# Kernel tuning notes

Measured on AMD Instinct MI355X. Metric: run time of the kernel, lower is better.

The kernel has to match this reference:

```python
import jax, jax.numpy as jnp
import numpy as np

B, S, L = 8, 2048, 8
H, NH = 768, 12
DH = H // NH
NUM_REL = 100
LN_EPS = 1e-5


def setup_inputs() -> dict:
    key = jax.random.key(0)
    ks = jax.random.split(key, 16)
    inp = {
        'text_embeddings': jax.random.normal(ks[0], (B, S, H), dtype=jnp.float32),
        # values in [-1, 64); -1 marks 'no leaf' and is masked out
        'graph_structure': jax.random.randint(ks[1], (B, S, L), -1, 64, dtype=jnp.int64),
        'relation_ids': jax.random.randint(ks[2], (B, S, L), 0, NUM_REL, dtype=jnp.int64),
        'rel_table': jax.random.normal(ks[3], (NUM_REL, H), dtype=jnp.float32),
        'Wq': jax.random.normal(ks[4], (H, H), dtype=jnp.float32) / np.sqrt(H),
        'bq': jnp.zeros((H,), dtype=jnp.float32),
        'Wk': jax.random.normal(ks[5], (H, H), dtype=jnp.float32) / np.sqrt(H),
        'bk': jnp.zeros((H,), dtype=jnp.float32),
        'Wv': jax.random.normal(ks[6], (H, H), dtype=jnp.float32) / np.sqrt(H),
        'bv': jnp.zeros((H,), dtype=jnp.float32),
        'Wo': jax.random.normal(ks[7], (H, H), dtype=jnp.float32) / np.sqrt(H),
        'bo': jnp.zeros((H,), dtype=jnp.float32),
        'gamma': jnp.ones((H,), dtype=jnp.float32),
        'beta': jnp.zeros((H,), dtype=jnp.float32),
    }
    return inp


def reference(text_embeddings, graph_structure, relation_ids, rel_table,
              Wq, bq, Wk, bk, Wv, bv, Wo, bo, gamma, beta):
    b, s, h = text_embeddings.shape
    l = relation_ids.shape[2]
    # embedding gather (clamp -1 -> 0, masked later)
    rel_emb = rel_table[jnp.clip(relation_ids, 0, None)]  # [B,S,L,H]
    # projections; query has length-1 per root token
    q = (text_embeddings @ Wq + bq).reshape(b, s, NH, DH)          # [B,S,N,D]
    k = (rel_emb @ Wk + bk).reshape(b, s, l, NH, DH)               # [B,S,L,N,D]
    v = (rel_emb @ Wv + bv).reshape(b, s, l, NH, DH)
    scores = jnp.einsum('bsnd,bslnd->bsnl', q, k) / np.sqrt(DH)    # [B,S,N,L]
    mask = (graph_structure != -1)[:, :, None, :]                  # [B,S,1,L]
    scores = jnp.where(mask, scores, jnp.float32(-10000.0))
    probs = jax.nn.softmax(scores, axis=-1)                        # [B,S,N,L]
    ctx = jnp.einsum('bsnl,bslnd->bsnd', probs, v).reshape(b, s, h)
    out = ctx @ Wo + bo
    x = text_embeddings + out
    mu = jnp.mean(x, axis=-1, keepdims=True)
    var = jnp.mean(jnp.square(x - mu), axis=-1, keepdims=True)
    return (x - mu) * jax.lax.rsqrt(var + LN_EPS) * gamma + beta
```

## Files before the change

### kernel.cpp

```cpp
#include <hip/hip_runtime.h>
#include <hip/hip_bf16.h>

#define H 768
#define NH 12
#define DH 64
#define LL 8
#define NTOK 16384
#define NREL 100
#define NRELP 128
#define PADW 72

typedef __attribute__((ext_vector_type(8))) short short8;
typedef __attribute__((ext_vector_type(4))) float f32x4;

__device__ __forceinline__ float bf2f(ushort u) {
  union { unsigned int i; float f; } v; v.i = ((unsigned int)u) << 16; return v.f;
}
__device__ __forceinline__ float bflo(unsigned int u) {
  union { unsigned int i; float f; } v; v.i = u << 16; return v.f;
}
__device__ __forceinline__ float bfhi(unsigned int u) {
  union { unsigned int i; float f; } v; v.i = u & 0xffff0000u; return v.f;
}
__device__ __forceinline__ ushort f2bf(float f) {
  union { float f; unsigned int i; } v; v.f = f;
  unsigned int x = v.i;
  return (ushort)((x + 0x7fffu + ((x >> 16) & 1u)) >> 16);
}
__device__ __forceinline__ unsigned int cvt_pk_bf16(float lo, float hi) {
  unsigned int r;
  asm("v_cvt_pk_bf16_f32 %0, %1, %2" : "=v"(r) : "v"(lo), "v"(hi));
  return r;
}

__global__ __launch_bounds__(256) void prep_kernel(
    const float* __restrict__ s0, ushort* __restrict__ d0,
    const float* __restrict__ s1, ushort* __restrict__ d1,
    const float* __restrict__ s2, ushort* __restrict__ d2,
    const float* __restrict__ s3, ushort* __restrict__ d3,
    const float* __restrict__ rel, ushort* __restrict__ RelB) {
  if (blockIdx.z == 4) {
    int b = blockIdx.y * 24 + blockIdx.x;
    if (b < 96) {
      int i = (b * 256 + threadIdx.x) * 4;
      int row = i / H;
      ushort4 o = {0, 0, 0, 0};
      if (row < NREL) {
        float4 v = *(const float4*)(rel + i);
        o.x = f2bf(v.x); o.y = f2bf(v.y); o.z = f2bf(v.z); o.w = f2bf(v.w);
      }
      *(ushort4*)(RelB + i) = o;
    }
    return;
  }
  const float* src; ushort* dst;
  switch (blockIdx.z) {
    case 0:  src = s0; dst = d0; break;
    case 1:  src = s1; dst = d1; break;
    case 2:  src = s2; dst = d2; break;
    default: src = s3; dst = d3; break;
  }
  __shared__ float tile[32][33];
  int bx = blockIdx.x * 32, by = blockIdx.y * 32;
  int tx = threadIdx.x & 31, ty = threadIdx.x >> 5;
  #pragma unroll
  for (int i = 0; i < 32; i += 8)
    tile[ty + i][tx] = src[(size_t)(by + ty + i) * H + bx + tx];
  __syncthreads();
  #pragma unroll
  for (int i = 0; i < 32; i += 8)
    dst[(size_t)(bx + ty + i) * H + by + tx] = f2bf(tile[tx][ty + i]);
}

__device__ __forceinline__ void gload_lds16(const void* g, void* l) {
  __builtin_amdgcn_global_load_lds(
      (const __attribute__((address_space(1))) unsigned int*)g,
      (__attribute__((address_space(3))) unsigned int*)l, 16, 0, 0);
}

#define BM 128
#define BN 256
#define BK 64
#define ATILE (BM * BK)
#define BTILE (BN * BK)

#define GEMM_COMPUTE()                                                         \
  _Pragma("unroll")                                                            \
  for (int kk = 0; kk < 2; ++kk) {                                             \
    const int sw = (((kk << 2) | lk) ^ (lr & 7)) * 8;                          \
    short8 af[4], bfr[8];                                                      \
    _Pragma("unroll")                                                          \
    for (int m = 0; m < 4; ++m)                                                \
      af[m] = *(const short8*)(As + (wr * 64 + m * 16 + lr) * BK + sw);        \
    _Pragma("unroll")                                                          \
    for (int n = 0; n < 8; ++n)                                                \
      bfr[n] = *(const short8*)(Bs + (wc * 128 + n * 16 + lr) * BK + sw);      \
    _Pragma("unroll")                                                          \
    for (int m = 0; m < 4; ++m)                                                \
      _Pragma("unroll")                                                        \
      for (int n = 0; n < 8; ++n)                                              \
        acc[m][n] = __builtin_amdgcn_mfma_f32_16x16x32_bf16(af[m], bfr[n],     \
                                                            acc[m][n], 0, 0, 0);\
  }

#define GEMM_EPILOGUE()                                                        \
  _Pragma("unroll")                                                            \
  for (int m = 0; m < 4; ++m) {                                                \
    _Pragma("unroll")                                                          \
    for (int n = 0; n < 8; ++n) {                                              \
      int col = col0 + wc * 128 + n * 16 + lr;                                 \
      float b = bias[col];                                                     \
      _Pragma("unroll")                                                        \
      for (int j = 0; j < 4; ++j) {                                            \
        int row = row0 + wr * 64 + m * 16 + lk * 4 + j;                        \
        C[(size_t)row * N + col] = f2bf(acc[m][n][j] + b);                     \
      }                                                                        \
    }                                                                          \
  }

__device__ __forceinline__ void gemm_body(
    ushort* As, ushort* Bs,
    const ushort* __restrict__ A,
    const ushort* __restrict__ Bt,
    const float* __restrict__ bias,
    ushort* __restrict__ C,
    int M, int N, int K, int bx, int by) {
  const int tid = threadIdx.x;
  const int row0 = by * BM;
  const int col0 = bx * BN;
  const int wave = tid >> 6;
  const int lane = tid & 63;
  const int wr = wave >> 1, wc = wave & 1;
  const int lr = lane & 15, lk = lane >> 4;
  f32x4 acc[4][8];
  #pragma unroll
  for (int m = 0; m < 4; ++m)
    #pragma unroll
    for (int n = 0; n < 8; ++n) acc[m][n] = (f32x4)(0.f);

  for (int k0 = 0; k0 < K; k0 += BK) {
    #pragma unroll
    for (int i = 0; i < 4; ++i) {
      int c = tid + i * 256; int r = c >> 3, s = c & 7; int gsx = s ^ (r & 7);
      gload_lds16(A + (size_t)(row0 + r) * K + k0 + gsx * 8, (char*)As + c * 16);
    }
    #pragma unroll
    for (int i = 0; i < 8; ++i) {
      int c = tid + i * 256; int r = c >> 3, s = c & 7; int gsx = s ^ (r & 7);
      gload_lds16(Bt + (size_t)(col0 + r) * K + k0 + gsx * 8, (char*)Bs + c * 16);
    }
    __syncthreads();
    GEMM_COMPUTE()
    __syncthreads();
  }
  GEMM_EPILOGUE()
}

__device__ __forceinline__ void gemm_body_a32(
    ushort* As, ushort* Bs,
    const float* __restrict__ A32,
    const ushort* __restrict__ Bt,
    const float* __restrict__ bias,
    ushort* __restrict__ C,
    int M, int N, int K, int bx, int by) {
  const int tid = threadIdx.x;
  const int row0 = by * BM;
  const int col0 = bx * BN;
  const int wave = tid >> 6;
  const int lane = tid & 63;
  const int wr = wave >> 1, wc = wave & 1;
  const int lr = lane & 15, lk = lane >> 4;
  f32x4 acc[4][8];
  #pragma unroll
  for (int m = 0; m < 4; ++m)
    #pragma unroll
    for (int n = 0; n < 8; ++n) acc[m][n] = (f32x4)(0.f);

  for (int k0 = 0; k0 < K; k0 += BK) {
    #pragma unroll
    for (int i = 0; i < 8; ++i) {
      int c = tid + i * 256; int r = c >> 3, s = c & 7; int gsx = s ^ (r & 7);
      gload_lds16(Bt + (size_t)(col0 + r) * K + k0 + gsx * 8, (char*)Bs + c * 16);
    }
    #pragma unroll
    for (int i = 0; i < 4; ++i) {
      int c = tid + i * 256; int r = c >> 3, s = c & 7; int gsx = s ^ (r & 7);
      const float* src = A32 + (size_t)(row0 + r) * K + k0 + gsx * 8;
      float4 f0 = *(const float4*)(src);
      float4 f1 = *(const float4*)(src + 4);
      uint4 w;
      w.x = cvt_pk_bf16(f0.x, f0.y);
      w.y = cvt_pk_bf16(f0.z, f0.w);
      w.z = cvt_pk_bf16(f1.x, f1.y);
      w.w = cvt_pk_bf16(f1.z, f1.w);
      *(uint4*)((char*)As + c * 16) = w;
    }
    __syncthreads();
    GEMM_COMPUTE()
    __syncthreads();
  }
  GEMM_EPILOGUE()
}

__global__ __launch_bounds__(256, 2) void gemm_q_kv_kernel(
    const float* __restrict__ X, const ushort* __restrict__ WqT,
    const float* __restrict__ bq, ushort* __restrict__ Qbf,
    const ushort* __restrict__ RelB,
    const ushort* __restrict__ WkT, const float* __restrict__ bk, ushort* __restrict__ Ktab,
    const ushort* __restrict__ WvT, const float* __restrict__ bv, ushort* __restrict__ Vtab) {
  __shared__ ushort As[ATILE];
  __shared__ ushort Bs[BTILE];
  int lin = blockIdx.x;
  if (lin < 6) {
    if (lin < 3)
      gemm_body(As, Bs, RelB, WkT, bk, Ktab, NRELP, H, H, lin, 0);
    else
      gemm_body(As, Bs, RelB, WvT, bv, Vtab, NRELP, H, H, lin - 3, 0);
    return;
  }
  int l2 = lin - 6;
  int wg = (l2 & 7) * 48 + (l2 >> 3);
  gemm_body_a32(As, Bs, X, WqT, bq, Qbf, NTOK, H, H, wg % 3, wg / 3);
}

__global__ __launch_bounds__(256, 2) void gemm_bt_kernel(
    const ushort* __restrict__ A, const ushort* __restrict__ Bt,
    const float* __restrict__ bias, ushort* __restrict__ C,
    int M, int N, int K) {
  __shared__ ushort As[ATILE];
  __shared__ ushort Bs[BTILE];
  int lin = blockIdx.y * gridDim.x + blockIdx.x;
  int q = (gridDim.x * gridDim.y) >> 3;
  int wg = (lin & 7) * q + (lin >> 3);
  gemm_body(As, Bs, A, Bt, bias, C, M, N, K, wg % gridDim.x, wg / gridDim.x);
}

__global__ __launch_bounds__(256) void attn3_kernel(
    const ushort* __restrict__ Q,
    const ushort* __restrict__ Ktab,
    const ushort* __restrict__ Vtab,
    const int* __restrict__ graph,
    const int* __restrict__ relid,
    ushort* __restrict__ Ctx) {
  __shared__ __align__(16) ushort Ks[NREL * PADW];
  __shared__ __align__(16) ushort Vs[NREL * PADW];
  const int tid = threadIdx.x;
  const int head = blockIdx.y;
  const int t = blockIdx.x * 256 + tid;

  #pragma unroll
  for (int i = 0; i < 4; ++i) {
    int c = tid + i * 256;
    if (c < NREL * 9) {
      int row = c / 9, slot = c - row * 9;
      int gsx = (slot < 8) ? slot * 8 : 0;
      const size_t src = (size_t)row * H + head * DH + gsx;
      gload_lds16(Ktab + src, (char*)Ks + (size_t)c * 16);
      gload_lds16(Vtab + src, (char*)Vs + (size_t)c * 16);
    }
  }

  const uint4* qp = (const uint4*)(Q + (size_t)t * H + head * DH);
  uint4 qw[8];
  #pragma unroll
  for (int j = 0; j < 8; ++j) qw[j] = qp[j];
  const int4* gp = (const int4*)(graph + (size_t)t * LL);
  const int4* rp = (const int4*)(relid + (size_t)t * LL);
  int4 ga = gp[0], gb = gp[1];
  int4 ra = rp[0], rb = rp[1];
  int gs[8] = {ga.x, ga.y, ga.z, ga.w, gb.x, gb.y, gb.z, gb.w};
  int rid[8] = {ra.x, ra.y, ra.z, ra.w, rb.x, rb.y, rb.z, rb.w};
  int koff[8];
  #pragma unroll
  for (int l = 0; l < 8; ++l) {
    int r = rid[l] < 0 ? 0 : rid[l];
    koff[l] = r * (PADW * 2);
  }

  __syncthreads();

  float s[8];
  #pragma unroll
  for (int l = 0; l < 8; ++l) s[l] = 0.f;
  #pragma unroll
  for (int j = 0; j < 8; ++j) {
    float qf[8];
    qf[0] = bflo(qw[j].x); qf[1] = bfhi(qw[j].x);
    qf[2] = bflo(qw[j].y); qf[3] = bfhi(qw[j].y);
    qf[4] = bflo(qw[j].z); qf[5] = bfhi(qw[j].z);
    qf[6] = bflo(qw[j].w); qf[7] = bfhi(qw[j].w);
    #pragma unroll
    for (int l = 0; l < 8; ++l) {
      uint4 kw = *(const uint4*)((const char*)Ks + koff[l] + j * 16);
      s[l] += qf[0] * bflo(kw.x) + qf[1] * bfhi(kw.x)
            + qf[2] * bflo(kw.y) + qf[3] * bfhi(kw.y)
            + qf[4] * bflo(kw.z) + qf[5] * bfhi(kw.z)
            + qf[6] * bflo(kw.w) + qf[7] * bfhi(kw.w);
    }
  }

  #pragma unroll
  for (int l = 0; l < 8; ++l)
    s[l] = (gs[l] != -1) ? s[l] * 0.125f : -10000.0f;
  float mx = s[0];
  #pragma unroll
  for (int l = 1; l < 8; ++l) mx = fmaxf(mx, s[l]);
  float p[8], den = 0.f;
  #pragma unroll
  for (int l = 0; l < 8; ++l) { p[l] = __expf(s[l] - mx); den += p[l]; }
  float inv = 1.f / den;
  #pragma unroll
  for (int l = 0; l < 8; ++l) p[l] *= inv;

  ushort* cp = Ctx + (size_t)t * H + head * DH;
  #pragma unroll
  for (int j = 0; j < 8; ++j) {
    float a[8];
    #pragma unroll
    for (int d = 0; d < 8; ++d) a[d] = 0.f;
    #pragma unroll
    for (int l = 0; l < 8; ++l) {
      uint4 vw = *(const uint4*)((const char*)Vs + koff[l] + j * 16);
      a[0] += p[l] * bflo(vw.x); a[1] += p[l] * bfhi(vw.x);
      a[2] += p[l] * bflo(vw.y); a[3] += p[l] * bfhi(vw.y);
      a[4] += p[l] * bflo(vw.z); a[5] += p[l] * bfhi(vw.z);
      a[6] += p[l] * bflo(vw.w); a[7] += p[l] * bfhi(vw.w);
    }
    short8 o;
    #pragma unroll
    for (int d = 0; d < 8; ++d) o[d] = (short)f2bf(a[d]);
    *(short8*)(cp + j * 8) = o;
  }
}

__global__ __launch_bounds__(192) void ln_kernel(
    const float* __restrict__ text, const ushort* __restrict__ op,
    const float* __restrict__ gamma, const float* __restrict__ beta,
    float* __restrict__ out) {
  int t = blockIdx.x;
  int c0 = threadIdx.x * 4;
  float4 tv = *(const float4*)(text + (size_t)t * H + c0);
  ushort4 ov = *(const ushort4*)(op + (size_t)t * H + c0);
  float x0 = tv.x + bf2f(ov.x), x1 = tv.y + bf2f(ov.y);
  float x2 = tv.z + bf2f(ov.z), x3 = tv.w + bf2f(ov.w);
  float s = x0 + x1 + x2 + x3;
  float s2 = x0 * x0 + x1 * x1 + x2 * x2 + x3 * x3;
  #pragma unroll
  for (int off = 32; off > 0; off >>= 1) {
    s  += __shfl_xor(s, off, 64);
    s2 += __shfl_xor(s2, off, 64);
  }
  __shared__ float red[2][3];
  int wave = threadIdx.x >> 6, lane = threadIdx.x & 63;
  if (lane == 0) { red[0][wave] = s; red[1][wave] = s2; }
  __syncthreads();
  s  = red[0][0] + red[0][1] + red[0][2];
  s2 = red[1][0] + red[1][1] + red[1][2];
  float mu = s * (1.f / H);
  float var = s2 * (1.f / H) - mu * mu;
  float rs = rsqrtf(var + 1e-5f);
  float4 g4 = *(const float4*)(gamma + c0);
  float4 b4 = *(const float4*)(beta + c0);
  float4 o4;
  o4.x = (x0 - mu) * rs * g4.x + b4.x;
  o4.y = (x1 - mu) * rs * g4.y + b4.y;
  o4.z = (x2 - mu) * rs * g4.z + b4.z;
  o4.w = (x3 - mu) * rs * g4.w + b4.w;
  *(float4*)(out + (size_t)t * H + c0) = o4;
}

extern "C" void kernel_launch(void* const* d_in, const int* in_sizes, int n_in,
                              void* d_out, int out_size, void* d_ws, size_t ws_size,
                              hipStream_t stream) {
  const float* text      = (const float*)d_in[0];
  const int*   graph     = (const int*)d_in[1];
  const int*   relid     = (const int*)d_in[2];
  const float* rel_table = (const float*)d_in[3];
  const float* Wq = (const float*)d_in[4];  const float* bq = (const float*)d_in[5];
  const float* Wk = (const float*)d_in[6];  const float* bk = (const float*)d_in[7];
  const float* Wv = (const float*)d_in[8];  const float* bv = (const float*)d_in[9];
  const float* Wo = (const float*)d_in[10]; const float* bo = (const float*)d_in[11];
  const float* gamma = (const float*)d_in[12];
  const float* beta  = (const float*)d_in[13];
  float* out = (float*)d_out;
  char* ws = (char*)d_ws;

  const size_t TOKH = (size_t)NTOK * H;
  size_t off = 0;
  ushort* Ctx  = (ushort*)(ws + off); off += TOKH * 2;
  ushort* Qbf  = (ushort*)(ws + off); off += TOKH * 2;
  ushort* WqT  = (ushort*)(ws + off); off += (size_t)H * H * 2;
  ushort* WoT  = (ushort*)(ws + off); off += (size_t)H * H * 2;
  ushort* WkT  = (ushort*)(ws + off); off += (size_t)H * H * 2;
  ushort* WvT  = (ushort*)(ws + off); off += (size_t)H * H * 2;
  ushort* RelB = (ushort*)(ws + off); off += (size_t)NRELP * H * 2;
  ushort* Ktab = (ushort*)(ws + off); off += (size_t)NRELP * H * 2;
  ushort* Vtab = (ushort*)(ws + off); off += (size_t)NRELP * H * 2;

  prep_kernel<<<dim3(24, 24, 5), 256, 0, stream>>>(
      Wq, WqT, Wo, WoT, Wk, WkT, Wv, WvT, rel_table, RelB);
  gemm_q_kv_kernel<<<6 + 384, 256, 0, stream>>>(
      text, WqT, bq, Qbf, RelB, WkT, bk, Ktab, WvT, bv, Vtab);
  dim3 ga(NTOK / 256, NH);
  attn3_kernel<<<ga, 256, 0, stream>>>(Qbf, Ktab, Vtab, graph, relid, Ctx);
  dim3 g1(H / BN, NTOK / BM);
  gemm_bt_kernel<<<g1, 256, 0, stream>>>(Ctx, WoT, bo, Qbf, NTOK, H, H);
  ln_kernel<<<NTOK, 192, 0, stream>>>(text, Qbf, gamma, beta, out);
}
```

Baseline: 101.8 us.

## Fuse Q projection GEMM with relation attention to avoid Q round trip

Splits the K/V table GEMM into its own small kernel and fuses the Q projection GEMM with the per-token attention. Each 128x256 Q tile is staged as bf16 in shared memory (swizzled) and consumed right away for 4 heads, so Q is never written to or reread from global memory. In exchange the K/V table rows are now read straight from global/L2 instead of padded LDS copies, the fused kernel adds extra barriers, and only 256 threads handle 128 tokens x 4 heads, which serializes the attention phase inside the GEMM block.

After: 165.5 us. 1.63x slower.

```diff
diff --git a/kernel.cpp b/kernel.cpp
--- a/kernel.cpp
+++ b/kernel.cpp
@@ -8,7 +8,6 @@
 #define NTOK 16384
 #define NREL 100
 #define NRELP 128
-#define PADW 72
 
 typedef __attribute__((ext_vector_type(8))) short short8;
 typedef __attribute__((ext_vector_type(4))) float f32x4;
@@ -156,18 +155,35 @@
   GEMM_EPILOGUE()
 }
 
-__device__ __forceinline__ void gemm_body_a32(
-    ushort* As, ushort* Bs,
-    const float* __restrict__ A32,
-    const ushort* __restrict__ Bt,
-    const float* __restrict__ bias,
-    ushort* __restrict__ C,
-    int M, int N, int K, int bx, int by) {
+__global__ __launch_bounds__(256, 2) void kv_kernel(
+    const ushort* __restrict__ RelB,
+    const ushort* __restrict__ WkT, const float* __restrict__ bk, ushort* __restrict__ Ktab,
+    const ushort* __restrict__ WvT, const float* __restrict__ bv, ushort* __restrict__ Vtab) {
+  __shared__ ushort As[ATILE];
+  __shared__ ushort Bs[BTILE];
+  int lin = blockIdx.x;
+  if (lin < 3)
+    gemm_body(As, Bs, RelB, WkT, bk, Ktab, NRELP, H, H, lin, 0);
+  else
+    gemm_body(As, Bs, RelB, WvT, bv, Vtab, NRELP, H, H, lin - 3, 0);
+}
+
+__global__ __launch_bounds__(256, 2) void qattn_kernel(
+    const float* __restrict__ X, const ushort* __restrict__ WqT,
+    const float* __restrict__ bq,
+    const ushort* __restrict__ Ktab, const ushort* __restrict__ Vtab,
+    const int* __restrict__ graph, const int* __restrict__ relid,
+    ushort* __restrict__ Ctx) {
+  __shared__ ushort As[ATILE];
+  __shared__ ushort Bs[BTILE];
+  char* Qc = (char*)Bs;
   const int tid = threadIdx.x;
+  int lin = blockIdx.x;
+  int wg = (lin & 7) * 48 + (lin >> 3);
+  const int bx = wg % 3, by = wg / 3;
   const int row0 = by * BM;
   const int col0 = bx * BN;
-  const int wave = tid >> 6;
-  const int lane = tid & 63;
+  const int wave = tid >> 6, lane = tid & 63;
   const int wr = wave >> 1, wc = wave & 1;
   const int lr = lane & 15, lk = lane >> 4;
   f32x4 acc[4][8];
@@ -176,16 +192,16 @@
     #pragma unroll
     for (int n = 0; n < 8; ++n) acc[m][n] = (f32x4)(0.f);
 
-  for (int k0 = 0; k0 < K; k0 += BK) {
+  for (int k0 = 0; k0 < H; k0 += BK) {
     #pragma unroll
     for (int i = 0; i < 8; ++i) {
       int c = tid + i * 256; int r = c >> 3, s = c & 7; int gsx = s ^ (r & 7);
-      gload_lds16(Bt + (size_t)(col0 + r) * K + k0 + gsx * 8, (char*)Bs + c * 16);
+      gload_lds16(WqT + (size_t)(col0 + r) * H + k0 + gsx * 8, (char*)Bs + c * 16);
     }
     #pragma unroll
     for (int i = 0; i < 4; ++i) {
       int c = tid + i * 256; int r = c >> 3, s = c & 7; int gsx = s ^ (r & 7);
-      const float* src = A32 + (size_t)(row0 + r) * K + k0 + gsx * 8;
+      const float* src = X + (size_t)(row0 + r) * H + k0 + gsx * 8;
       float4 f0 = *(const float4*)(src);
       float4 f1 = *(const float4*)(src + 4);
       uint4 w;
@@ -199,28 +215,110 @@
     GEMM_COMPUTE()
     __syncthreads();
   }
-  GEMM_EPILOGUE()
-}
-
-__global__ __launch_bounds__(256, 2) void gemm_q_kv_kernel(
-    const float* __restrict__ X, const ushort* __restrict__ WqT,
-    const float* __restrict__ bq, ushort* __restrict__ Qbf,
-    const ushort* __restrict__ RelB,
-    const ushort* __restrict__ WkT, const float* __restrict__ bk, ushort* __restrict__ Ktab,
-    const ushort* __restrict__ WvT, const float* __restrict__ bv, ushort* __restrict__ Vtab) {
-  __shared__ ushort As[ATILE];
-  __shared__ ushort Bs[BTILE];
-  int lin = blockIdx.x;
-  if (lin < 6) {
-    if (lin < 3)
-      gemm_body(As, Bs, RelB, WkT, bk, Ktab, NRELP, H, H, lin, 0);
-    else
-      gemm_body(As, Bs, RelB, WvT, bv, Vtab, NRELP, H, H, lin - 3, 0);
-    return;
-  }
-  int l2 = lin - 6;
-  int wg = (l2 & 7) * 48 + (l2 >> 3);
-  gemm_body_a32(As, Bs, X, WqT, bq, Qbf, NTOK, H, H, wg % 3, wg / 3);
+
+  unsigned int pk[4][8][2];
+  #pragma unroll
+  for (int m = 0; m < 4; ++m)
+    #pragma unroll
+    for (int n = 0; n < 8; ++n) {
+      float b = bq[col0 + wc * 128 + n * 16 + lr];
+      pk[m][n][0] = cvt_pk_bf16(acc[m][n][0] + b, acc[m][n][1] + b);
+      pk[m][n][1] = cvt_pk_bf16(acc[m][n][2] + b, acc[m][n][3] + b);
+    }
+
+  #pragma unroll
+  for (int h2 = 0; h2 < 2; ++h2) {
+    if (wc == h2) {
+      #pragma unroll
+      for (int m = 0; m < 4; ++m)
+        #pragma unroll
+        for (int n = 0; n < 8; ++n) {
+          int colc = n * 16 + lr;
+          int ch = colc >> 3;
+          #pragma unroll
+          for (int j = 0; j < 4; ++j) {
+            int trow = wr * 64 + m * 16 + lk * 4 + j;
+            unsigned int u = pk[m][n][j >> 1];
+            ushort val = (j & 1) ? (ushort)(u >> 16) : (ushort)(u & 0xffffu);
+            *(ushort*)(Qc + trow * 256 + ((ch ^ (trow & 15)) << 4)
+                       + ((colc & 7) << 1)) = val;
+          }
+        }
+    }
+    __syncthreads();
+    {
+      const int hh = tid & 1, t = tid >> 1;
+      const int head = bx * 4 + h2 * 2 + hh;
+      const int gtok = row0 + t;
+      uint4 qw[8];
+      #pragma unroll
+      for (int k = 0; k < 8; ++k)
+        qw[k] = *(const uint4*)(Qc + t * 256 + ((((hh << 3) | k) ^ (t & 15)) << 4));
+      const int4* gp = (const int4*)(graph + (size_t)gtok * LL);
+      const int4* rp = (const int4*)(relid + (size_t)gtok * LL);
+      int4 ga = gp[0], gb = gp[1];
+      int4 ra = rp[0], rb = rp[1];
+      int gs[8] = {ga.x, ga.y, ga.z, ga.w, gb.x, gb.y, gb.z, gb.w};
+      int rid[8] = {ra.x, ra.y, ra.z, ra.w, rb.x, rb.y, rb.z, rb.w};
+      size_t koff[8];
+      #pragma unroll
+      for (int l = 0; l < 8; ++l) {
+        int r = rid[l] < 0 ? 0 : rid[l];
+        koff[l] = (size_t)r * H + head * DH;
+      }
+      float s[8];
+      #pragma unroll
+      for (int l = 0; l < 8; ++l) s[l] = 0.f;
+      #pragma unroll
+      for (int j = 0; j < 8; ++j) {
+        float qf[8];
+        qf[0] = bflo(qw[j].x); qf[1] = bfhi(qw[j].x);
+        qf[2] = bflo(qw[j].y); qf[3] = bfhi(qw[j].y);
+        qf[4] = bflo(qw[j].z); qf[5] = bfhi(qw[j].z);
+        qf[6] = bflo(qw[j].w); qf[7] = bfhi(qw[j].w);
+        #pragma unroll
+        for (int l = 0; l < 8; ++l) {
+          uint4 kw = *(const uint4*)(Ktab + koff[l] + j * 8);
+          s[l] += qf[0] * bflo(kw.x) + qf[1] * bfhi(kw.x)
+                + qf[2] * bflo(kw.y) + qf[3] * bfhi(kw.y)
+                + qf[4] * bflo(kw.z) + qf[5] * bfhi(kw.z)
+                + qf[6] * bflo(kw.w) + qf[7] * bfhi(kw.w);
+        }
+      }
+      #pragma unroll
+      for (int l = 0; l < 8; ++l)
+        s[l] = (gs[l] != -1) ? s[l] * 0.125f : -10000.0f;
+      float mx = s[0];
+      #pragma unroll
+      for (int l = 1; l < 8; ++l) mx = fmaxf(mx, s[l]);
+      float p[8], den = 0.f;
+      #pragma unroll
+      for (int l = 0; l < 8; ++l) { p[l] = __expf(s[l] - mx); den += p[l]; }
+      float inv = 1.f / den;
+      #pragma unroll
+      for (int l = 0; l < 8; ++l) p[l] *= inv;
+      ushort* cp = Ctx + (size_t)gtok * H + head * DH;
+      #pragma unroll
+      for (int j = 0; j < 8; ++j) {
+        float a[8];
+        #pragma unroll
+        for (int d = 0; d < 8; ++d) a[d] = 0.f;
+        #pragma unroll
+        for (int l = 0; l < 8; ++l) {
+          uint4 vw = *(const uint4*)(Vtab + koff[l] + j * 8);
+          a[0] += p[l] * bflo(vw.x); a[1] += p[l] * bfhi(vw.x);
+          a[2] += p[l] * bflo(vw.y); a[3] += p[l] * bfhi(vw.y);
+          a[4] += p[l] * bflo(vw.z); a[5] += p[l] * bfhi(vw.z);
+          a[6] += p[l] * bflo(vw.w); a[7] += p[l] * bfhi(vw.w);
+        }
+        short8 o;
+        #pragma unroll
+        for (int d = 0; d < 8; ++d) o[d] = (short)f2bf(a[d]);
+        *(short8*)(cp + j * 8) = o;
+      }
+    }
+    __syncthreads();
+  }
 }
 
 __global__ __launch_bounds__(256, 2) void gemm_bt_kernel(
@@ -233,104 +331,6 @@
   int q = (gridDim.x * gridDim.y) >> 3;
   int wg = (lin & 7) * q + (lin >> 3);
   gemm_body(As, Bs, A, Bt, bias, C, M, N, K, wg % gridDim.x, wg / gridDim.x);
-}
-
-__global__ __launch_bounds__(256) void attn3_kernel(
-    const ushort* __restrict__ Q,
-    const ushort* __restrict__ Ktab,
-    const ushort* __restrict__ Vtab,
-    const int* __restrict__ graph,
-    const int* __restrict__ relid,
-    ushort* __restrict__ Ctx) {
-  __shared__ __align__(16) ushort Ks[NREL * PADW];
-  __shared__ __align__(16) ushort Vs[NREL * PADW];
-  const int tid = threadIdx.x;
-  const int head = blockIdx.y;
-  const int t = blockIdx.x * 256 + tid;
-
-  #pragma unroll
-  for (int i = 0; i < 4; ++i) {
-    int c = tid + i * 256;
-    if (c < NREL * 9) {
-      int row = c / 9, slot = c - row * 9;
-      int gsx = (slot < 8) ? slot * 8 : 0;
-      const size_t src = (size_t)row * H + head * DH + gsx;
-      gload_lds16(Ktab + src, (char*)Ks + (size_t)c * 16);
-      gload_lds16(Vtab + src, (char*)Vs + (size_t)c * 16);
-    }
-  }
-
-  const uint4* qp = (const uint4*)(Q + (size_t)t * H + head * DH);
-  uint4 qw[8];
-  #pragma unroll
-  for (int j = 0; j < 8; ++j) qw[j] = qp[j];
-  const int4* gp = (const int4*)(graph + (size_t)t * LL);
-  const int4* rp = (const int4*)(relid + (size_t)t * LL);
-  int4 ga = gp[0], gb = gp[1];
-  int4 ra = rp[0], rb = rp[1];
-  int gs[8] = {ga.x, ga.y, ga.z, ga.w, gb.x, gb.y, gb.z, gb.w};
-  int rid[8] = {ra.x, ra.y, ra.z, ra.w, rb.x, rb.y, rb.z, rb.w};
-  int koff[8];
-  #pragma unroll
-  for (int l = 0; l < 8; ++l) {
-    int r = rid[l] < 0 ? 0 : rid[l];
-    koff[l] = r * (PADW * 2);
-  }
-
-  __syncthreads();
-
-  float s[8];
-  #pragma unroll
-  for (int l = 0; l < 8; ++l) s[l] = 0.f;
-  #pragma unroll
-  for (int j = 0; j < 8; ++j) {
-    float qf[8];
-    qf[0] = bflo(qw[j].x); qf[1] = bfhi(qw[j].x);
-    qf[2] = bflo(qw[j].y); qf[3] = bfhi(qw[j].y);
-    qf[4] = bflo(qw[j].z); qf[5] = bfhi(qw[j].z);
-    qf[6] = bflo(qw[j].w); qf[7] = bfhi(qw[j].w);
-    #pragma unroll
-    for (int l = 0; l < 8; ++l) {
-      uint4 kw = *(const uint4*)((const char*)Ks + koff[l] + j * 16);
-      s[l] += qf[0] * bflo(kw.x) + qf[1] * bfhi(kw.x)
-            + qf[2] * bflo(kw.y) + qf[3] * bfhi(kw.y)
-            + qf[4] * bflo(kw.z) + qf[5] * bfhi(kw.z)
-            + qf[6] * bflo(kw.w) + qf[7] * bfhi(kw.w);
-    }
-  }
-
-  #pragma unroll
-  for (int l = 0; l < 8; ++l)
-    s[l] = (gs[l] != -1) ? s[l] * 0.125f : -10000.0f;
-  float mx = s[0];
-  #pragma unroll
-  for (int l = 1; l < 8; ++l) mx = fmaxf(mx, s[l]);
-  float p[8], den = 0.f;
-  #pragma unroll
-  for (int l = 0; l < 8; ++l) { p[l] = __expf(s[l] - mx); den += p[l]; }
-  float inv = 1.f / den;
-  #pragma unroll
-  for (int l = 0; l < 8; ++l) p[l] *= inv;
-
-  ushort* cp = Ctx + (size_t)t * H + head * DH;
-  #pragma unroll
-  for (int j = 0; j < 8; ++j) {
-    float a[8];
-    #pragma unroll
-    for (int d = 0; d < 8; ++d) a[d] = 0.f;
-    #pragma unroll
-    for (int l = 0; l < 8; ++l) {
-      uint4 vw = *(const uint4*)((const char*)Vs + koff[l] + j * 16);
-      a[0] += p[l] * bflo(vw.x); a[1] += p[l] * bfhi(vw.x);
-      a[2] += p[l] * bflo(vw.y); a[3] += p[l] * bfhi(vw.y);
-      a[4] += p[l] * bflo(vw.z); a[5] += p[l] * bfhi(vw.z);
-      a[6] += p[l] * bflo(vw.w); a[7] += p[l] * bfhi(vw.w);
-    }
-    short8 o;
-    #pragma unroll
-    for (int d = 0; d < 8; ++d) o[d] = (short)f2bf(a[d]);
-    *(short8*)(cp + j * 8) = o;
-  }
 }
 
 __global__ __launch_bounds__(192) void ln_kernel(
@@ -388,7 +388,7 @@
   const size_t TOKH = (size_t)NTOK * H;
   size_t off = 0;
   ushort* Ctx  = (ushort*)(ws + off); off += TOKH * 2;
-  ushort* Qbf  = (ushort*)(ws + off); off += TOKH * 2;
+  ushort* OP   = (ushort*)(ws + off); off += TOKH * 2;
   ushort* WqT  = (ushort*)(ws + off); off += (size_t)H * H * 2;
   ushort* WoT  = (ushort*)(ws + off); off += (size_t)H * H * 2;
   ushort* WkT  = (ushort*)(ws + off); off += (size_t)H * H * 2;
@@ -399,11 +399,10 @@
 
   prep_kernel<<<dim3(24, 24, 5), 256, 0, stream>>>(
       Wq, WqT, Wo, WoT, Wk, WkT, Wv, WvT, rel_table, RelB);
-  gemm_q_kv_kernel<<<6 + 384, 256, 0, stream>>>(
-      text, WqT, bq, Qbf, RelB, WkT, bk, Ktab, WvT, bv, Vtab);
-  dim3 ga(NTOK / 256, NH);
-  attn3_kernel<<<ga, 256, 0, stream>>>(Qbf, Ktab, Vtab, graph, relid, Ctx);
+  kv_kernel<<<6, 256, 0, stream>>>(RelB, WkT, bk, Ktab, WvT, bv, Vtab);
+  qattn_kernel<<<384, 256, 0, stream>>>(
+      text, WqT, bq, Ktab, Vtab, graph, relid, Ctx);
   dim3 g1(H / BN, NTOK / BM);
-  gemm_bt_kernel<<<g1, 256, 0, stream>>>(Ctx, WoT, bo, Qbf, NTOK, H, H);
-  ln_kernel<<<NTOK, 192, 0, stream>>>(text, Qbf, gamma, beta, out);
-}
+  gemm_bt_kernel<<<g1, 256, 0, stream>>>(Ctx, WoT, bo, OP, NTOK, H, H);
+  ln_kernel<<<NTOK, 192, 0, stream>>>(text, OP, gamma, beta, out);
+}
```
